# Kernel tuning notes

Measured on AMD Instinct MI355X. Metric: run time of the kernel, lower is better.

Reference implementation:

```python
import jax, jax.numpy as jnp
import numpy as np

EPS = 1e-5
B, HD, LD, OD, E = 4, 256, 512, 256, 64  # E = out_dim // reduction
H, W, H2, W2 = 64, 64, 32, 32

def conv1x1(x, Wt, b=None):
    # x: [B,C,H,W], Wt: [O,C]
    y = jnp.einsum('bchw,oc->bohw', x, Wt)
    if b is not None:
        y = y + b[None, :, None, None]
    return y

def bn(x, s, bi, m, v):
    # eval-mode BatchNorm2d with running stats
    inv = (s / jnp.sqrt(v + EPS))[None, :, None, None]
    return (x - m[None, :, None, None]) * inv + bi[None, :, None, None]

def setup_inputs() -> dict:
    key = jax.random.key(0)
    ks = jax.random.split(key, 24)
    def n(k, shape, scale=0.05):
        return jax.random.normal(k, shape, dtype=jnp.float32) * scale
    inp = {
        'high_feat': jax.random.normal(ks[0], (B, HD, H, W), dtype=jnp.float32),
        'low_feat': jax.random.normal(ks[1], (B, LD, H2, W2), dtype=jnp.float32),
        'W_high': n(ks[2], (E, HD)),
        'bn_h_scale': 1.0 + n(ks[3], (E,)), 'bn_h_bias': n(ks[4], (E,)),
        'bn_h_mean': n(ks[5], (E,)), 'bn_h_var': 0.5 + jax.random.uniform(ks[6], (E,), dtype=jnp.float32),
        'W_low': n(ks[7], (E, LD)),
        'bn_l_scale': 1.0 + n(ks[8], (E,)), 'bn_l_bias': n(ks[9], (E,)),
        'bn_l_mean': n(ks[10], (E,)), 'bn_l_var': 0.5 + jax.random.uniform(ks[11], (E,), dtype=jnp.float32),
        'W_q': n(ks[12], (E, E)), 'b_q': n(ks[13], (E,)),
        'W_k': n(ks[14], (E, E)), 'b_k': n(ks[15], (E,)),
        'W_vh': n(ks[16], (OD, HD)), 'b_vh': n(ks[17], (OD,)),
        'W_vl': n(ks[18], (OD, LD)), 'b_vl': n(ks[19], (OD,)),
        'W_out': n(ks[20], (OD, 2 * OD)),
        'bn_o_scale': 1.0 + n(ks[21], (OD,)), 'bn_o_bias': n(ks[22], (OD,)),
        'bn_o_mean': jnp.zeros((OD,), jnp.float32), 'bn_o_var': jnp.ones((OD,), jnp.float32),
        'gamma': n(ks[23], (1,), scale=0.5),
    }
    return inp

def reference(high_feat, low_feat, W_high, bn_h_scale, bn_h_bias, bn_h_mean, bn_h_var,
              W_low, bn_l_scale, bn_l_bias, bn_l_mean, bn_l_var,
              W_q, b_q, W_k, b_k, W_vh, b_vh, W_vl, b_vl,
              W_out, bn_o_scale, bn_o_bias, bn_o_mean, bn_o_var, gamma):
    N = H * W
    # bilinear upsample low_feat to high_feat spatial size (align_corners=False)
    low = jax.image.resize(low_feat, (B, LD, H, W), method='bilinear')
    he = jax.nn.relu(bn(conv1x1(high_feat, W_high), bn_h_scale, bn_h_bias, bn_h_mean, bn_h_var))
    le = jax.nn.relu(bn(conv1x1(low, W_low), bn_l_scale, bn_l_bias, bn_l_mean, bn_l_var))
    q = conv1x1(he, W_q, b_q).reshape(B, E, N)   # [B,E,N1]
    k = conv1x1(le, W_k, b_k).reshape(B, E, N)   # [B,E,N2]
    energy = jnp.einsum('bcn,bcm->bnm', q, k)    # [B,N1,N2]
    attn = jax.nn.softmax(energy, axis=-1)
    vh = conv1x1(high_feat, W_vh, b_vh).reshape(B, OD, N)
    vl = conv1x1(low, W_vl, b_vl).reshape(B, OD, N)
    out_high = jnp.einsum('bcm,bnm->bcn', vh, attn).reshape(B, OD, H, W)
    out_low = jnp.einsum('bcn,bnm->bcm', vl, attn).reshape(B, OD, H, W)
    cat = jnp.concatenate([out_high, out_low], axis=1)  # [B,2*OD,H,W]
    out = jax.nn.relu(bn(conv1x1(cat, W_out), bn_o_scale, bn_o_bias, bn_o_mean, bn_o_var))
    return high_feat + gamma[0] * out
```

## Files before the change

kernel.cpp:

```cpp
#include <hip/hip_runtime.h>
#include <hip/hip_bf16.h>

#define B_   4
#define HD_  256
#define LD_  512
#define OD_  256
#define E_   64
#define N_   4096
#define N2_  1024
#define EPS_ 1e-5f

typedef __hip_bfloat16 bf16;
typedef __attribute__((ext_vector_type(8))) short short8;
typedef __attribute__((ext_vector_type(4))) float floatx4;

#define MFMA16(a, b, c) __builtin_amdgcn_mfma_f32_16x16x32_bf16(a, b, c, 0, 0, 0)

#define GLOAD(dst, ptr) \
  asm volatile("global_load_dwordx4 %0, %1, off" : "=v"(dst) : "v"(ptr) : "memory")
#define VWAIT() do { \
  asm volatile("s_waitcnt vmcnt(0)" ::: "memory"); \
  __builtin_amdgcn_sched_barrier(0); \
} while (0)

#define WH_OFF   0
#define WL_OFF   16384
#define WQ_OFF   49152
#define WK_OFF   53248
#define WVH_OFF  57344
#define WVL_OFF  122880
#define WO_OFF   253952
#define WTOT     385024

__device__ __forceinline__ unsigned short f2b_bits(float f) {
  union { float f; unsigned int u; } cv; cv.f = f;
  unsigned int u = cv.u;
  return (unsigned short)((u + 0x7FFFu + ((u >> 16) & 1u)) >> 16);
}
__device__ __forceinline__ float bits2f(unsigned short h) {
  union { unsigned int u; float f; } cv; cv.u = ((unsigned int)h) << 16;
  return cv.f;
}
__device__ __forceinline__ float ldext(const void* p, size_t i, int fl) {
  if (fl) return __bfloat162float(((const bf16*)p)[i]);
  return ((const float*)p)[i];
}
__device__ __forceinline__ short8 ld8(const short* p) { return *(const short8*)p; }
__device__ __forceinline__ short8 i4s8(int4 v) {
  union { int4 i; short8 s; } u; u.i = v; return u.s;
}
__device__ __forceinline__ short8 ldP(const unsigned short* row, int off) {
  ushort4 a = *(const ushort4*)(row + off);
  ushort4 b = *(const ushort4*)(row + off + 4);
  short8 r;
  r[0] = (short)a.x; r[1] = (short)a.y; r[2] = (short)a.z; r[3] = (short)a.w;
  r[4] = (short)b.x; r[5] = (short)b.y; r[6] = (short)b.z; r[7] = (short)b.w;
  return r;
}

__device__ __forceinline__ size_t qk_off(int n, int e) {
  return ((size_t)(n >> 4) << 10) + ((e >> 5) << 9) + ((n & 15) << 5) + (e & 31);
}
__device__ __forceinline__ size_t v_off(int c, int m) {
  return ((size_t)(m >> 5) << 13) + ((c >> 4) << 9) + (((m >> 3) & 3) << 7)
       + ((c & 15) << 3) + (m & 7);
}
__device__ __forceinline__ size_t o_off(int n, int c) {
  return ((size_t)(n >> 4) << 12) + ((c >> 5) << 9) + ((n & 15) << 5) + (c & 31);
}

__global__ void detect_dtype_k(const void* probe, int* dflag) {
  if (threadIdx.x == 0 && blockIdx.x == 0) {
    const unsigned int* u = (const unsigned int*)probe;
    int bf = 1;
    for (int i = 0; i < 32; i++)
      if (u[i] != 0x3F803F80u) bf = 0;
    dflag[0] = bf;
  }
}

__global__ __launch_bounds__(256) void cvt_weights_k(
    const void* Wh, const void* Wl, const void* Wq, const void* Wk,
    const void* Wvh, const void* Wvl, const void* Wo,
    unsigned short* wbuf, const int* dflag)
{
  const int fl = dflag[0];
  int i = blockIdx.x * 256 + threadIdx.x;
  if (i >= WTOT) return;
  const void* src; int li;
  if      (i < WL_OFF)  { src = Wh;  li = i - WH_OFF;  }
  else if (i < WQ_OFF)  { src = Wl;  li = i - WL_OFF;  }
  else if (i < WK_OFF)  { src = Wq;  li = i - WQ_OFF;  }
  else if (i < WVH_OFF) { src = Wk;  li = i - WK_OFF;  }
  else if (i < WVL_OFF) { src = Wvh; li = i - WVH_OFF; }
  else if (i < WO_OFF)  { src = Wvl; li = i - WVL_OFF; }
  else                  { src = Wo;  li = i - WO_OFF;  }
  wbuf[i] = f2b_bits(ldext(src, li, fl));
}

__global__ __launch_bounds__(256) void transpose_cvt_k(
    const void* X, unsigned short* Xt, int C, int S, const int* dflag)
{
  __shared__ unsigned short T[64][66];
  const int fl = dflag[0];
  const int tid = threadIdx.x;
  const int s0 = blockIdx.x * 64, c0 = blockIdx.y * 64, b = blockIdx.z;
  const size_t ibase = (size_t)b * C * S;
  const size_t obase = (size_t)b * S * C;
  const int sl = tid & 63, q = tid >> 6;
  for (int i = 0; i < 16; i++) {
    int c = q + i * 4;
    T[c][sl] = f2b_bits(ldext(X, ibase + (size_t)(c0 + c) * S + s0 + sl, fl));
  }
  __syncthreads();
  for (int i = 0; i < 16; i++) {
    int s = q + i * 4;
    Xt[obase + (size_t)(s0 + s) * C + c0 + sl] = T[sl][s];
  }
}

__global__ __launch_bounds__(256) void gemm_k(
    const unsigned short* A, long sA, int lda,
    const unsigned short* Bm, long sB, int ldb,
    unsigned short* D, long sD, int ldd,
    int K, int mode, int axis, int swz,
    const void* p0, const void* p1, const void* p2, const void* p3,
    const int* dflag)
{
  const int fl = dflag[0];
  const int tid = threadIdx.x;
  const int w = tid >> 6, lane = tid & 63;
  const int g = lane >> 4, c16 = lane & 15;
  const int r0 = blockIdx.x * 64 + (w >> 1) * 32;
  const int c0 = blockIdx.y * 64 + (w & 1) * 32;
  const short* Ab = (const short*)A + (size_t)blockIdx.z * sA;
  const short* Bb = (const short*)Bm + (size_t)blockIdx.z * sB;
  unsigned short* Db = D + (size_t)blockIdx.z * sD;

  floatx4 acc[2][2];
  #pragma unroll
  for (int i = 0; i < 2; i++)
    #pragma unroll
    for (int j = 0; j < 2; j++) acc[i][j] = (floatx4){0.f, 0.f, 0.f, 0.f};

  for (int k0 = 0; k0 < K; k0 += 64) {
    short8 Af[2][2], Bf[2][2];
    #pragma unroll
    for (int t = 0; t < 2; t++)
      #pragma unroll
      for (int kc = 0; kc < 2; kc++) {
        Af[t][kc] = ld8(Ab + (size_t)(r0 + t * 16 + c16) * lda + k0 + kc * 32 + g * 8);
        Bf[t][kc] = ld8(Bb + (size_t)(c0 + t * 16 + c16) * ldb + k0 + kc * 32 + g * 8);
      }
    #pragma unroll
    for (int kc = 0; kc < 2; kc++)
      #pragma unroll
      for (int rt = 0; rt < 2; rt++)
        #pragma unroll
        for (int ct = 0; ct < 2; ct++)
          acc[rt][ct] = MFMA16(Af[rt][kc], Bf[ct][kc], acc[rt][ct]);
  }

  #pragma unroll
  for (int rt = 0; rt < 2; rt++)
    #pragma unroll
    for (int ct = 0; ct < 2; ct++)
      #pragma unroll
      for (int r = 0; r < 4; r++) {
        int rr = r0 + rt * 16 + g * 4 + r;
        int cc = c0 + ct * 16 + c16;
        int pi = axis ? rr : cc;
        float v = acc[rt][ct][r];
        if (mode == 1) v += ldext(p0, pi, fl);
        else if (mode >= 2) {
          float inv = ldext(p0, pi, fl) * rsqrtf(ldext(p3, pi, fl) + EPS_);
          v = v * inv + (ldext(p1, pi, fl) - ldext(p2, pi, fl) * inv);
          if (mode == 3) v = fmaxf(v, 0.f);
        }
        size_t idx;
        if (swz == 1)      idx = qk_off(rr, cc);
        else if (swz == 2) idx = v_off(rr, cc);
        else               idx = (size_t)rr * ldd + cc;
        Db[idx] = f2b_bits(v);
      }
}

__global__ __launch_bounds__(256) void upsample_rows_k(
    const unsigned short* src, unsigned short* dst, int relu)
{
  int idx = blockIdx.x * 256 + threadIdx.x;
  int e = idx & 63, n = (idx >> 6) & (N_ - 1), b = idx >> 18;
  int y = n >> 6, x = n & 63;
  int y0 = (y - 1) >> 1;  float wy = (y & 1) ? 0.25f : 0.75f;
  int x0 = (x - 1) >> 1;  float wx = (x & 1) ? 0.25f : 0.75f;
  int y0c = max(y0, 0), y1c = min(y0 + 1, 31);
  int x0c = max(x0, 0), x1c = min(x0 + 1, 31);
  const unsigned short* sb = src + ((size_t)b * N2_) * 64 + e;
  float v00 = bits2f(sb[(y0c * 32 + x0c) * 64]), v01 = bits2f(sb[(y0c * 32 + x1c) * 64]);
  float v10 = bits2f(sb[(y1c * 32 + x0c) * 64]), v11 = bits2f(sb[(y1c * 32 + x1c) * 64]);
  float v = (1.f - wy) * ((1.f - wx) * v00 + wx * v01)
          + wy * ((1.f - wx) * v10 + wx * v11);
  if (relu) v = fmaxf(v, 0.f);
  dst[idx] = f2b_bits(v);
}

__global__ __launch_bounds__(256) void upsample_swz_k(
    const unsigned short* src, unsigned short* dst)
{
  int idx = blockIdx.x * 256 + threadIdx.x;
  int n = idx & (N_ - 1), c = (idx >> 12) & 255, b = idx >> 20;
  int y = n >> 6, x = n & 63;
  int y0 = (y - 1) >> 1;  float wy = (y & 1) ? 0.25f : 0.75f;
  int x0 = (x - 1) >> 1;  float wx = (x & 1) ? 0.25f : 0.75f;
  int y0c = max(y0, 0), y1c = min(y0 + 1, 31);
  int x0c = max(x0, 0), x1c = min(x0 + 1, 31);
  const unsigned short* sb = src + (size_t)(b * 256 + c) * N2_;
  float v00 = bits2f(sb[y0c * 32 + x0c]), v01 = bits2f(sb[y0c * 32 + x1c]);
  float v10 = bits2f(sb[y1c * 32 + x0c]), v11 = bits2f(sb[y1c * 32 + x1c]);
  float v = (1.f - wy) * ((1.f - wx) * v00 + wx * v01)
          + wy * ((1.f - wx) * v10 + wx * v11);
  dst[(size_t)b * 256 * N_ + v_off(c, n)] = f2b_bits(v);
}


__global__ __launch_bounds__(256, 4) void attn_apply_high_mfma_k(
    const bf16* qt, const bf16* kt, const bf16* vh,
    float* lsum_p, unsigned short* ohp0, unsigned short* ohp1)
{
  __shared__ __align__(16) unsigned short Pb[2][32][132];
  __shared__ float Lw[4][32];
  const int tid = threadIdx.x;
  const int w = tid >> 6, lane = tid & 63;
  const int g = lane >> 4, c16 = lane & 15;
  const int L = blockIdx.x;
  const int b = (L & 7) >> 1;
  const int n0 = (L >> 3) * 32;
  const int half = L & 1;
  const int mbase = half * 2048, mend = mbase + 2048;
  const short* q = (const short*)qt + (size_t)b * N_ * E_;
  const short* k = (const short*)kt + (size_t)b * N_ * E_;
  const short* v = (const short*)vh + (size_t)b * OD_ * N_;

  short8 Aq[2][2];
  #pragma unroll
  for (int nt = 0; nt < 2; nt++)
    #pragma unroll
    for (int ks = 0; ks < 2; ks++)
      Aq[nt][ks] = ld8(q + qk_off(n0 + nt * 16 + c16, ks * 32 + g * 8));

  float lsum[2][4] = {};
  floatx4 oacc[2][4];
  #pragma unroll
  for (int nt = 0; nt < 2; nt++)
    #pragma unroll
    for (int ct = 0; ct < 4; ct++)
      oacc[nt][ct] = (floatx4){0.f, 0.f, 0.f, 0.f};

  short8 BkC[2][2];
  #pragma unroll
  for (int mt = 0; mt < 2; mt++)
    #pragma unroll
    for (int ks = 0; ks < 2; ks++)
      BkC[mt][ks] = ld8(k + qk_off(mbase + w * 32 + mt * 16 + c16, ks * 32 + g * 8));

  int buf = 0;
  for (int m0 = mbase; m0 < mend; m0 += 128, buf ^= 1) {
    int4 bv[8];
    #pragma unroll
    for (int ks = 0; ks < 2; ks++)
      #pragma unroll
      for (int ct = 0; ct < 4; ct++)
        GLOAD(bv[ks * 4 + ct],
              (v + v_off(w * 64 + ct * 16 + c16, m0 + ks * 32 + g * 8)));
    floatx4 s[2][2];
    #pragma unroll
    for (int nt = 0; nt < 2; nt++)
      #pragma unroll
      for (int mt = 0; mt < 2; mt++) {
        floatx4 z = (floatx4){0.f, 0.f, 0.f, 0.f};
        z = MFMA16(Aq[nt][0], BkC[mt][0], z);
        z = MFMA16(Aq[nt][1], BkC[mt][1], z);
        s[nt][mt] = z;
      }
    int mn_ = m0 + 128;
    if (mn_ < mend) {
      #pragma unroll
      for (int mt = 0; mt < 2; mt++)
        #pragma unroll
        for (int ks = 0; ks < 2; ks++)
          BkC[mt][ks] = ld8(k + qk_off(mn_ + w * 32 + mt * 16 + c16, ks * 32 + g * 8));
    }
    #pragma unroll
    for (int nt = 0; nt < 2; nt++)
      #pragma unroll
      for (int mt = 0; mt < 2; mt++)
        #pragma unroll
        for (int r = 0; r < 4; r++) {
          float p = __expf(fminf(s[nt][mt][r], 60.f));
          lsum[nt][r] += p;
          Pb[buf][nt * 16 + g * 4 + r][w * 32 + mt * 16 + c16] = f2b_bits(p);
        }
    __syncthreads();
    VWAIT();
    #pragma unroll
    for (int ks = 0; ks < 2; ks++) {
      short8 Ap0 = ldP(&Pb[buf][c16][0],      ks * 32 + g * 8);
      short8 Ap1 = ldP(&Pb[buf][16 + c16][0], ks * 32 + g * 8);
      #pragma unroll
      for (int ct = 0; ct < 4; ct++) {
        short8 Bv = i4s8(bv[ks * 4 + ct]);
        oacc[0][ct] = MFMA16(Ap0, Bv, oacc[0][ct]);
        oacc[1][ct] = MFMA16(Ap1, Bv, oacc[1][ct]);
      }
    }
    #pragma unroll
    for (int ks = 0; ks < 2; ks++)
      #pragma unroll
      for (int ct = 0; ct < 4; ct++)
        GLOAD(bv[ks * 4 + ct],
              (v + v_off(w * 64 + ct * 16 + c16, m0 + (ks + 2) * 32 + g * 8)));
    VWAIT();
    #pragma unroll
    for (int ks = 0; ks < 2; ks++) {
      short8 Ap0 = ldP(&Pb[buf][c16][0],      (ks + 2) * 32 + g * 8);
      short8 Ap1 = ldP(&Pb[buf][16 + c16][0], (ks + 2) * 32 + g * 8);
      #pragma unroll
      for (int ct = 0; ct < 4; ct++) {
        short8 Bv = i4s8(bv[ks * 4 + ct]);
        oacc[0][ct] = MFMA16(Ap0, Bv, oacc[0][ct]);
        oacc[1][ct] = MFMA16(Ap1, Bv, oacc[1][ct]);
      }
    }
  }
  #pragma unroll
  for (int d = 1; d < 16; d <<= 1)
    #pragma unroll
    for (int nt = 0; nt < 2; nt++)
      #pragma unroll
      for (int r = 0; r < 4; r++)
        lsum[nt][r] += __shfl_xor(lsum[nt][r], d);
  if (c16 == 0)
    #pragma unroll
    for (int nt = 0; nt < 2; nt++)
      #pragma unroll
      for (int r = 0; r < 4; r++)
        Lw[w][nt * 16 + g * 4 + r] = lsum[nt][r];
  __syncthreads();
  if (tid < 32)
    lsum_p[(size_t)half * 16384 + (size_t)b * N_ + n0 + tid] =
        Lw[0][tid] + Lw[1][tid] + Lw[2][tid] + Lw[3][tid];
  unsigned short* op = (half ? ohp1 : ohp0) + (size_t)b * N_ * OD_;
  #pragma unroll
  for (int nt = 0; nt < 2; nt++)
    #pragma unroll
    for (int ct = 0; ct < 4; ct++)
      #pragma unroll
      for (int r = 0; r < 4; r++) {
        int n = n0 + nt * 16 + g * 4 + r;
        int c = w * 64 + ct * 16 + c16;
        op[o_off(n, c)] = f2b_bits(oacc[nt][ct][r]);
      }
}

__global__ __launch_bounds__(256) void reduce_high_k(
    const unsigned short* p0, const unsigned short* p1, const float* lsum_p,
    unsigned short* oh, float* rsumG)
{
  size_t i8 = ((size_t)blockIdx.x * 256 + threadIdx.x) * 8;
  int slab = (int)(i8 >> 20);
  int loc  = (int)(i8 & 0xFFFFF);
  int n = (loc >> 12) * 16 + ((loc >> 5) & 15);
  int row = slab * N_ + n;
  float l = lsum_p[row] + lsum_p[16384 + row];
  float ri = 1.0f / l;
  const unsigned short* a = p0 + i8;
  const unsigned short* b = p1 + i8;
  short8 o;
  #pragma unroll
  for (int i = 0; i < 8; i++)
    o[i] = (short)f2b_bits((bits2f(a[i]) + bits2f(b[i])) * ri);
  *(short8*)(oh + i8) = o;
  if ((loc & 31) == 0) rsumG[row] = l;
}

__global__ __launch_bounds__(256, 4) void attn_apply_low_mfma_k(
    const bf16* qt, const bf16* kt, const bf16* vl,
    const float* rsumG, unsigned short* olp0, unsigned short* olp1)
{
  __shared__ __align__(16) unsigned short Pb[2][32][132];
  const int tid = threadIdx.x;
  const int w = tid >> 6, lane = tid & 63;
  const int g = lane >> 4, c16 = lane & 15;
  const int L = blockIdx.x;
  const int b = (L & 7) >> 1;
  const int m0 = (L >> 3) * 32;
  const int half = L & 1;
  const int nbase = half * 2048, nend = nbase + 2048;
  const short* q = (const short*)qt + (size_t)b * N_ * E_;
  const short* k = (const short*)kt + (size_t)b * N_ * E_;
  const short* v = (const short*)vl + (size_t)b * OD_ * N_;

  short8 Ak[2][2];
  #pragma unroll
  for (int mt = 0; mt < 2; mt++)
    #pragma unroll
    for (int ks = 0; ks < 2; ks++)
      Ak[mt][ks] = ld8(k + qk_off(m0 + mt * 16 + c16, ks * 32 + g * 8));

  floatx4 oacc[2][4];
  #pragma unroll
  for (int mt = 0; mt < 2; mt++)
    #pragma unroll
    for (int ct = 0; ct < 4; ct++)
      oacc[mt][ct] = (floatx4){0.f, 0.f, 0.f, 0.f};

  short8 BqC[2][2];
  float riC[2];
  #pragma unroll
  for (int nt = 0; nt < 2; nt++) {
    #pragma unroll
    for (int ks = 0; ks < 2; ks++)
      BqC[nt][ks] = ld8(q + qk_off(nbase + w * 32 + nt * 16 + c16, ks * 32 + g * 8));
    riC[nt] = 1.0f / rsumG[(size_t)b * N_ + nbase + w * 32 + nt * 16 + c16];
  }

  int buf = 0;
  for (int nL = nbase; nL < nend; nL += 128, buf ^= 1) {
    int4 bv[8];
    #pragma unroll
    for (int ks = 0; ks < 2; ks++)
      #pragma unroll
      for (int ct = 0; ct < 4; ct++)
        GLOAD(bv[ks * 4 + ct],
              (v + v_off(w * 64 + ct * 16 + c16, nL + ks * 32 + g * 8)));
    floatx4 s[2][2];
    #pragma unroll
    for (int mt = 0; mt < 2; mt++)
      #pragma unroll
      for (int nt = 0; nt < 2; nt++) {
        floatx4 z = (floatx4){0.f, 0.f, 0.f, 0.f};
        z = MFMA16(Ak[mt][0], BqC[nt][0], z);
        z = MFMA16(Ak[mt][1], BqC[nt][1], z);
        s[mt][nt] = z;
      }
    float riU[2]; riU[0] = riC[0]; riU[1] = riC[1];
    int nn_ = nL + 128;
    if (nn_ < nend) {
      #pragma unroll
      for (int nt = 0; nt < 2; nt++) {
        #pragma unroll
        for (int ks = 0; ks < 2; ks++)
          BqC[nt][ks] = ld8(q + qk_off(nn_ + w * 32 + nt * 16 + c16, ks * 32 + g * 8));
        riC[nt] = 1.0f / rsumG[(size_t)b * N_ + nn_ + w * 32 + nt * 16 + c16];
      }
    }
    #pragma unroll
    for (int mt = 0; mt < 2; mt++)
      #pragma unroll
      for (int nt = 0; nt < 2; nt++)
        #pragma unroll
        for (int r = 0; r < 4; r++)
          Pb[buf][mt * 16 + g * 4 + r][w * 32 + nt * 16 + c16] =
              f2b_bits(__expf(fminf(s[mt][nt][r], 60.f)) * riU[nt]);
    __syncthreads();
    VWAIT();
    #pragma unroll
    for (int ks = 0; ks < 2; ks++) {
      short8 Ap0 = ldP(&Pb[buf][c16][0],      ks * 32 + g * 8);
      short8 Ap1 = ldP(&Pb[buf][16 + c16][0], ks * 32 + g * 8);
      #pragma unroll
      for (int ct = 0; ct < 4; ct++) {
        short8 Bv = i4s8(bv[ks * 4 + ct]);
        oacc[0][ct] = MFMA16(Ap0, Bv, oacc[0][ct]);
        oacc[1][ct] = MFMA16(Ap1, Bv, oacc[1][ct]);
      }
    }
    #pragma unroll
    for (int ks = 0; ks < 2; ks++)
      #pragma unroll
      for (int ct = 0; ct < 4; ct++)
        GLOAD(bv[ks * 4 + ct],
              (v + v_off(w * 64 + ct * 16 + c16, nL + (ks + 2) * 32 + g * 8)));
    VWAIT();
    #pragma unroll
    for (int ks = 0; ks < 2; ks++) {
      short8 Ap0 = ldP(&Pb[buf][c16][0],      (ks + 2) * 32 + g * 8);
      short8 Ap1 = ldP(&Pb[buf][16 + c16][0], (ks + 2) * 32 + g * 8);
      #pragma unroll
      for (int ct = 0; ct < 4; ct++) {
        short8 Bv = i4s8(bv[ks * 4 + ct]);
        oacc[0][ct] = MFMA16(Ap0, Bv, oacc[0][ct]);
        oacc[1][ct] = MFMA16(Ap1, Bv, oacc[1][ct]);
      }
    }
  }
  unsigned short* op = (half ? olp1 : olp0) + (size_t)b * N_ * OD_;
  #pragma unroll
  for (int mt = 0; mt < 2; mt++)
    #pragma unroll
    for (int ct = 0; ct < 4; ct++)
      #pragma unroll
      for (int r = 0; r < 4; r++) {
        int m = m0 + mt * 16 + g * 4 + r;
        int c = w * 64 + ct * 16 + c16;
        op[o_off(m, c)] = f2b_bits(oacc[mt][ct][r]);
      }
}

__global__ __launch_bounds__(256) void reduce_low_k(
    const unsigned short* p0, const unsigned short* p1, unsigned short* ol)
{
  size_t i8 = ((size_t)blockIdx.x * 256 + threadIdx.x) * 8;
  const unsigned short* a = p0 + i8;
  const unsigned short* b = p1 + i8;
  short8 o;
  #pragma unroll
  for (int i = 0; i < 8; i++)
    o[i] = (short)f2b_bits(bits2f(a[i]) + bits2f(b[i]));
  *(short8*)(ol + i8) = o;
}

__global__ __launch_bounds__(256) void final_mfma_k(
    const unsigned short* Wo, const unsigned short* oh, const unsigned short* ol,
    const void* sc, const void* bi, const void* mn, const void* vr,
    const void* hf, const void* gamma, void* out, const int* dflag)
{
  const int fl = dflag[0];
  const int tid = threadIdx.x;
  const int w = tid >> 6, lane = tid & 63;
  const int g = lane >> 4, c16 = lane & 15;
  const int r0 = blockIdx.x * 64 + (w >> 1) * 32;
  const int c0 = blockIdx.y * 64 + (w & 1) * 32;
  const int b = blockIdx.z;

  floatx4 acc[2][2];
  #pragma unroll
  for (int i = 0; i < 2; i++)
    #pragma unroll
    for (int j = 0; j < 2; j++) acc[i][j] = (floatx4){0.f, 0.f, 0.f, 0.f};

  #pragma unroll
  for (int half = 0; half < 2; half++) {
    const short* Bb = (const short*)(half ? ol : oh) + (size_t)b * N_ * 256;
    for (int k0 = 0; k0 < 256; k0 += 64) {
      short8 Af[2][2], Bf[2][2];
      #pragma unroll
      for (int t = 0; t < 2; t++)
        #pragma unroll
        for (int kc = 0; kc < 2; kc++) {
          Af[t][kc] = ld8((const short*)Wo + (size_t)(r0 + t * 16 + c16) * 512 +
                          half * 256 + k0 + kc * 32 + g * 8);
          Bf[t][kc] = ld8(Bb + o_off(c0 + t * 16 + c16, k0 + kc * 32 + g * 8));
        }
      #pragma unroll
      for (int kc = 0; kc < 2; kc++)
        #pragma unroll
        for (int rt = 0; rt < 2; rt++)
          #pragma unroll
          for (int ct = 0; ct < 2; ct++)
            acc[rt][ct] = MFMA16(Af[rt][kc], Bf[ct][kc], acc[rt][ct]);
    }
  }

  float gm = ldext(gamma, 0, fl);
  #pragma unroll
  for (int rt = 0; rt < 2; rt++)
    #pragma unroll
    for (int r = 0; r < 4; r++) {
      int o = r0 + rt * 16 + g * 4 + r;
      float inv = ldext(sc, o, fl) * rsqrtf(ldext(vr, o, fl) + EPS_);
      float bb = ldext(bi, o, fl) - ldext(mn, o, fl) * inv;
      #pragma unroll
      for (int ct = 0; ct < 2; ct++) {
        int n = c0 + ct * 16 + c16;
        float v = acc[rt][ct][r] * inv + bb;
        v = fmaxf(v, 0.f);
        size_t idx = ((size_t)b * OD_ + o) * N_ + n;
        float res = ldext(hf, idx, fl) + gm * v;
        if (fl) ((bf16*)out)[idx] = __float2bfloat16(res);
        else    ((float*)out)[idx] = res;
      }
    }
}

extern "C" void kernel_launch(void* const* d_in, const int* in_sizes, int n_in,
                              void* d_out, int out_size, void* d_ws, size_t ws_size,
                              hipStream_t stream)
{
  const void* hf     = d_in[0];
  const void* lf     = d_in[1];
  const void* W_high = d_in[2];
  const void* bhs = d_in[3],  *bhb = d_in[4],  *bhm = d_in[5],  *bhv = d_in[6];
  const void* W_low  = d_in[7];
  const void* bls = d_in[8],  *blb = d_in[9],  *blm = d_in[10], *blv = d_in[11];
  const void* W_q    = d_in[12], *b_q = d_in[13];
  const void* W_k    = d_in[14], *b_k = d_in[15];
  const void* W_vh   = d_in[16], *b_vh = d_in[17];
  const void* W_vl   = d_in[18], *b_vl = d_in[19];
  const void* W_out  = d_in[20];
  const void* bos = d_in[21], *bob = d_in[22], *bom = d_in[23], *bov = d_in[24];
  const void* gamma  = d_in[25];

  char* wp = (char*)d_ws;
  int*   dflag  = (int*)wp;                                 wp += 64;
  float* rsum   = (float*)wp;                               wp += 16384 * 4;
  float* lsum_p = (float*)wp;                               wp += 2 * 16384 * 4;
  unsigned short* wbuf  = (unsigned short*)wp;              wp += WTOT * 2;
  unsigned short* hf_t  = (unsigned short*)wp;              wp += (size_t)B_ * N_ * 256 * 2;
  unsigned short* lf_t  = (unsigned short*)wp;              wp += (size_t)B_ * N2_ * 512 * 2;
  unsigned short* he_t  = (unsigned short*)wp;              wp += (size_t)B_ * N_ * 64 * 2;
  unsigned short* le_sm = (unsigned short*)wp;              wp += (size_t)B_ * N2_ * 64 * 2;
  unsigned short* le_t  = (unsigned short*)wp;              wp += (size_t)B_ * N_ * 64 * 2;
  unsigned short* vl_sm = (unsigned short*)wp;              wp += (size_t)B_ * 256 * N2_ * 2;
  unsigned short* vh    = (unsigned short*)wp;              wp += (size_t)B_ * 256 * N_ * 2;
  unsigned short* vl    = (unsigned short*)wp;              wp += (size_t)B_ * 256 * N_ * 2;
  unsigned short* ol    = (unsigned short*)wp;              wp += (size_t)B_ * N_ * 256 * 2;
  unsigned short* pext  = (unsigned short*)wp;              wp += (size_t)B_ * N_ * 256 * 2;
  unsigned short* oh = hf_t;
  unsigned short* qv = lf_t;
  unsigned short* kv = lf_t + (size_t)B_ * N_ * 64;
  unsigned short* ohp0 = ol;
  unsigned short* ohp1 = pext;
  unsigned short* olp0 = vh;
  unsigned short* olp1 = pext;

  dim3 blk(256);
  detect_dtype_k<<<1, 64, 0, stream>>>(bov, dflag);
  cvt_weights_k<<<WTOT / 256, blk, 0, stream>>>(W_high, W_low, W_q, W_k, W_vh, W_vl, W_out,
                                                wbuf, dflag);
  transpose_cvt_k<<<dim3(64, 4, B_), blk, 0, stream>>>(hf, hf_t, 256, N_, dflag);
  transpose_cvt_k<<<dim3(16, 8, B_), blk, 0, stream>>>(lf, lf_t, 512, N2_, dflag);

  gemm_k<<<dim3(256, 1, 1), blk, 0, stream>>>(hf_t, 0, 256, wbuf + WH_OFF, 0, 256,
      he_t, 0, 64, 256, 3, 0, 0, bhs, bhb, bhm, bhv, dflag);
  gemm_k<<<dim3(4, 64, B_), blk, 0, stream>>>(wbuf + WVH_OFF, 0, 256,
      hf_t, (long)N_ * 256, 256, vh, (long)256 * N_, N_, 256, 1, 1, 2,
      b_vh, b_vh, b_vh, b_vh, dflag);
  gemm_k<<<dim3(64, 1, 1), blk, 0, stream>>>(lf_t, 0, 512, wbuf + WL_OFF, 0, 512,
      le_sm, 0, 64, 512, 2, 0, 0, bls, blb, blm, blv, dflag);
  gemm_k<<<dim3(4, 16, B_), blk, 0, stream>>>(wbuf + WVL_OFF, 0, 512,
      lf_t, (long)N2_ * 512, 512, vl_sm, (long)256 * N2_, N2_, 512, 1, 1, 0,
      b_vl, b_vl, b_vl, b_vl, dflag);
  upsample_rows_k<<<(B_ * N_ * 64) / 256, blk, 0, stream>>>(le_sm, le_t, 1);
  upsample_swz_k <<<(B_ * 256 * N_) / 256, blk, 0, stream>>>(vl_sm, vl);
  gemm_k<<<dim3(256, 1, 1), blk, 0, stream>>>(he_t, 0, 64, wbuf + WQ_OFF, 0, 64,
      qv, 0, 64, 64, 1, 0, 1, b_q, b_q, b_q, b_q, dflag);
  gemm_k<<<dim3(256, 1, 1), blk, 0, stream>>>(le_t, 0, 64, wbuf + WK_OFF, 0, 64,
      kv, 0, 64, 64, 1, 0, 1, b_k, b_k, b_k, b_k, dflag);

  attn_apply_high_mfma_k<<<dim3(1024), blk, 0, stream>>>((const bf16*)qv, (const bf16*)kv,
      (const bf16*)vh, lsum_p, ohp0, ohp1);
  reduce_high_k<<<dim3(2048), blk, 0, stream>>>(ohp0, ohp1, lsum_p, oh, rsum);
  attn_apply_low_mfma_k <<<dim3(1024), blk, 0, stream>>>((const bf16*)qv, (const bf16*)kv,
      (const bf16*)vl, rsum, olp0, olp1);
  reduce_low_k<<<dim3(2048), blk, 0, stream>>>(olp0, olp1, ol);

  final_mfma_k<<<dim3(4, 64, B_), blk, 0, stream>>>(wbuf + WO_OFF, oh, ol,
      bos, bob, bom, bov, hf, gamma, d_out, dflag);
}
```

Baseline: 399.1 us.

## Store all GEMM operands in MFMA fragment-tiled layout

Introduces a generic fragment-tiled layout (16-row by 32-k tiles stored contiguously) and uses it for the converted weights, the transposed inputs, the upsampled key features, the intermediate he tensor and the final-stage operands. Every gemm and MFMA kernel now loads operands through this layout, so each wave's 16-byte fragment loads hit contiguous memory rather than strided rows. The cost is scattered stores in the producer kernels (weight conversion, transpose, upsample) and more index arithmetic. It also risks layout mismatches between producers and consumers, such as le_sm, which is still written row-major and read by the upsample kernel.

```diff
diff --git a/kernel.cpp b/kernel.cpp
--- a/kernel.cpp
+++ b/kernel.cpp
@@ -58,15 +58,13 @@
   return r;
 }
 
-__device__ __forceinline__ size_t qk_off(int n, int e) {
-  return ((size_t)(n >> 4) << 10) + ((e >> 5) << 9) + ((n & 15) << 5) + (e & 31);
+__device__ __forceinline__ size_t frag_off(int r, int k, int K) {
+  return ((size_t)(r >> 4) * ((size_t)K << 4)) + ((size_t)(k >> 5) << 9)
+       + ((r & 15) << 5) + (k & 31);
 }
 __device__ __forceinline__ size_t v_off(int c, int m) {
   return ((size_t)(m >> 5) << 13) + ((c >> 4) << 9) + (((m >> 3) & 3) << 7)
        + ((c & 15) << 3) + (m & 7);
-}
-__device__ __forceinline__ size_t o_off(int n, int c) {
-  return ((size_t)(n >> 4) << 12) + ((c >> 5) << 9) + ((n & 15) << 5) + (c & 31);
 }
 
 __global__ void detect_dtype_k(const void* probe, int* dflag) {
@@ -87,15 +85,17 @@
   const int fl = dflag[0];
   int i = blockIdx.x * 256 + threadIdx.x;
   if (i >= WTOT) return;
-  const void* src; int li;
-  if      (i < WL_OFF)  { src = Wh;  li = i - WH_OFF;  }
-  else if (i < WQ_OFF)  { src = Wl;  li = i - WL_OFF;  }
-  else if (i < WK_OFF)  { src = Wq;  li = i - WQ_OFF;  }
-  else if (i < WVH_OFF) { src = Wk;  li = i - WK_OFF;  }
-  else if (i < WVL_OFF) { src = Wvh; li = i - WVH_OFF; }
-  else if (i < WO_OFF)  { src = Wvl; li = i - WVL_OFF; }
-  else                  { src = Wo;  li = i - WO_OFF;  }
-  wbuf[i] = f2b_bits(ldext(src, li, fl));
+  const void* src; int li, off, ksh;
+  if      (i < WL_OFF)  { src = Wh;  li = i - WH_OFF;  off = WH_OFF;  ksh = 8; }
+  else if (i < WQ_OFF)  { src = Wl;  li = i - WL_OFF;  off = WL_OFF;  ksh = 9; }
+  else if (i < WK_OFF)  { src = Wq;  li = i - WQ_OFF;  off = WQ_OFF;  ksh = 6; }
+  else if (i < WVH_OFF) { src = Wk;  li = i - WK_OFF;  off = WK_OFF;  ksh = 6; }
+  else if (i < WVL_OFF) { src = Wvh; li = i - WVH_OFF; off = WVH_OFF; ksh = 8; }
+  else if (i < WO_OFF)  { src = Wvl; li = i - WVL_OFF; off = WVL_OFF; ksh = 9; }
+  else                  { src = Wo;  li = i - WO_OFF;  off = WO_OFF;  ksh = 9; }
+  int K = 1 << ksh;
+  int r = li >> ksh, k = li & (K - 1);
+  wbuf[off + frag_off(r, k, K)] = f2b_bits(ldext(src, li, fl));
 }
 
 __global__ __launch_bounds__(256) void transpose_cvt_k(
@@ -115,13 +115,13 @@
   __syncthreads();
   for (int i = 0; i < 16; i++) {
     int s = q + i * 4;
-    Xt[obase + (size_t)(s0 + s) * C + c0 + sl] = T[sl][s];
+    Xt[obase + frag_off(s0 + s, c0 + sl, C)] = T[sl][s];
   }
 }
 
 __global__ __launch_bounds__(256) void gemm_k(
-    const unsigned short* A, long sA, int lda,
-    const unsigned short* Bm, long sB, int ldb,
+    const unsigned short* A, long sA,
+    const unsigned short* Bm, long sB,
     unsigned short* D, long sD, int ldd,
     int K, int mode, int axis, int swz,
     const void* p0, const void* p1, const void* p2, const void* p3,
@@ -149,8 +149,8 @@
     for (int t = 0; t < 2; t++)
       #pragma unroll
       for (int kc = 0; kc < 2; kc++) {
-        Af[t][kc] = ld8(Ab + (size_t)(r0 + t * 16 + c16) * lda + k0 + kc * 32 + g * 8);
-        Bf[t][kc] = ld8(Bb + (size_t)(c0 + t * 16 + c16) * ldb + k0 + kc * 32 + g * 8);
+        Af[t][kc] = ld8(Ab + frag_off(r0 + t * 16 + c16, k0 + kc * 32 + g * 8, K));
+        Bf[t][kc] = ld8(Bb + frag_off(c0 + t * 16 + c16, k0 + kc * 32 + g * 8, K));
       }
     #pragma unroll
     for (int kc = 0; kc < 2; kc++)
@@ -178,7 +178,7 @@
           if (mode == 3) v = fmaxf(v, 0.f);
         }
         size_t idx;
-        if (swz == 1)      idx = qk_off(rr, cc);
+        if (swz == 1)      idx = frag_off(rr, cc, ldd);
         else if (swz == 2) idx = v_off(rr, cc);
         else               idx = (size_t)rr * ldd + cc;
         Db[idx] = f2b_bits(v);
@@ -201,7 +201,7 @@
   float v = (1.f - wy) * ((1.f - wx) * v00 + wx * v01)
           + wy * ((1.f - wx) * v10 + wx * v11);
   if (relu) v = fmaxf(v, 0.f);
-  dst[idx] = f2b_bits(v);
+  dst[(size_t)b * N_ * 64 + frag_off(n, e, 64)] = f2b_bits(v);
 }
 
 __global__ __launch_bounds__(256) void upsample_swz_k(
@@ -246,7 +246,7 @@
   for (int nt = 0; nt < 2; nt++)
     #pragma unroll
     for (int ks = 0; ks < 2; ks++)
-      Aq[nt][ks] = ld8(q + qk_off(n0 + nt * 16 + c16, ks * 32 + g * 8));
+      Aq[nt][ks] = ld8(q + frag_off(n0 + nt * 16 + c16, ks * 32 + g * 8, 64));
 
   float lsum[2][4] = {};
   floatx4 oacc[2][4];
@@ -261,7 +261,7 @@
   for (int mt = 0; mt < 2; mt++)
     #pragma unroll
     for (int ks = 0; ks < 2; ks++)
-      BkC[mt][ks] = ld8(k + qk_off(mbase + w * 32 + mt * 16 + c16, ks * 32 + g * 8));
+      BkC[mt][ks] = ld8(k + frag_off(mbase + w * 32 + mt * 16 + c16, ks * 32 + g * 8, 64));
 
   int buf = 0;
   for (int m0 = mbase; m0 < mend; m0 += 128, buf ^= 1) {
@@ -288,7 +288,7 @@
       for (int mt = 0; mt < 2; mt++)
         #pragma unroll
         for (int ks = 0; ks < 2; ks++)
-          BkC[mt][ks] = ld8(k + qk_off(mn_ + w * 32 + mt * 16 + c16, ks * 32 + g * 8));
+          BkC[mt][ks] = ld8(k + frag_off(mn_ + w * 32 + mt * 16 + c16, ks * 32 + g * 8, 64));
     }
     #pragma unroll
     for (int nt = 0; nt < 2; nt++)
@@ -358,7 +358,7 @@
       for (int r = 0; r < 4; r++) {
         int n = n0 + nt * 16 + g * 4 + r;
         int c = w * 64 + ct * 16 + c16;
-        op[o_off(n, c)] = f2b_bits(oacc[nt][ct][r]);
+        op[frag_off(n, c, 256)] = f2b_bits(oacc[nt][ct][r]);
       }
 }
 
@@ -405,7 +405,7 @@
   for (int mt = 0; mt < 2; mt++)
     #pragma unroll
     for (int ks = 0; ks < 2; ks++)
-      Ak[mt][ks] = ld8(k + qk_off(m0 + mt * 16 + c16, ks * 32 + g * 8));
+      Ak[mt][ks] = ld8(k + frag_off(m0 + mt * 16 + c16, ks * 32 + g * 8, 64));
 
   floatx4 oacc[2][4];
   #pragma unroll
@@ -420,7 +420,7 @@
   for (int nt = 0; nt < 2; nt++) {
     #pragma unroll
     for (int ks = 0; ks < 2; ks++)
-      BqC[nt][ks] = ld8(q + qk_off(nbase + w * 32 + nt * 16 + c16, ks * 32 + g * 8));
+      BqC[nt][ks] = ld8(q + frag_off(nbase + w * 32 + nt * 16 + c16, ks * 32 + g * 8, 64));
     riC[nt] = 1.0f / rsumG[(size_t)b * N_ + nbase + w * 32 + nt * 16 + c16];
   }
 
@@ -450,7 +450,7 @@
       for (int nt = 0; nt < 2; nt++) {
         #pragma unroll
         for (int ks = 0; ks < 2; ks++)
-          BqC[nt][ks] = ld8(q + qk_off(nn_ + w * 32 + nt * 16 + c16, ks * 32 + g * 8));
+          BqC[nt][ks] = ld8(q + frag_off(nn_ + w * 32 + nt * 16 + c16, ks * 32 + g * 8, 64));
         riC[nt] = 1.0f / rsumG[(size_t)b * N_ + nn_ + w * 32 + nt * 16 + c16];
       }
     }
@@ -503,7 +503,7 @@
       for (int r = 0; r < 4; r++) {
         int m = m0 + mt * 16 + g * 4 + r;
         int c = w * 64 + ct * 16 + c16;
-        op[o_off(m, c)] = f2b_bits(oacc[mt][ct][r]);
+        op[frag_off(m, c, 256)] = f2b_bits(oacc[mt][ct][r]);
       }
 }
 
@@ -548,9 +548,9 @@
       for (int t = 0; t < 2; t++)
         #pragma unroll
         for (int kc = 0; kc < 2; kc++) {
-          Af[t][kc] = ld8((const short*)Wo + (size_t)(r0 + t * 16 + c16) * 512 +
-                          half * 256 + k0 + kc * 32 + g * 8);
-          Bf[t][kc] = ld8(Bb + o_off(c0 + t * 16 + c16, k0 + kc * 32 + g * 8));
+          Af[t][kc] = ld8((const short*)Wo + frag_off(r0 + t * 16 + c16,
+                          half * 256 + k0 + kc * 32 + g * 8, 512));
+          Bf[t][kc] = ld8(Bb + frag_off(c0 + t * 16 + c16, k0 + kc * 32 + g * 8, 256));
         }
       #pragma unroll
       for (int kc = 0; kc < 2; kc++)
@@ -631,21 +631,21 @@
   transpose_cvt_k<<<dim3(64, 4, B_), blk, 0, stream>>>(hf, hf_t, 256, N_, dflag);
   transpose_cvt_k<<<dim3(16, 8, B_), blk, 0, stream>>>(lf, lf_t, 512, N2_, dflag);
 
-  gemm_k<<<dim3(256, 1, 1), blk, 0, stream>>>(hf_t, 0, 256, wbuf + WH_OFF, 0, 256,
-      he_t, 0, 64, 256, 3, 0, 0, bhs, bhb, bhm, bhv, dflag);
-  gemm_k<<<dim3(4, 64, B_), blk, 0, stream>>>(wbuf + WVH_OFF, 0, 256,
-      hf_t, (long)N_ * 256, 256, vh, (long)256 * N_, N_, 256, 1, 1, 2,
+  gemm_k<<<dim3(256, 1, 1), blk, 0, stream>>>(hf_t, 0, wbuf + WH_OFF, 0,
+      he_t, 0, 64, 256, 3, 0, 1, bhs, bhb, bhm, bhv, dflag);
+  gemm_k<<<dim3(4, 64, B_), blk, 0, stream>>>(wbuf + WVH_OFF, 0,
+      hf_t, (long)N_ * 256, vh, (long)256 * N_, N_, 256, 1, 1, 2,
       b_vh, b_vh, b_vh, b_vh, dflag);
-  gemm_k<<<dim3(64, 1, 1), blk, 0, stream>>>(lf_t, 0, 512, wbuf + WL_OFF, 0, 512,
+  gemm_k<<<dim3(64, 1, 1), blk, 0, stream>>>(lf_t, 0, wbuf + WL_OFF, 0,
       le_sm, 0, 64, 512, 2, 0, 0, bls, blb, blm, blv, dflag);
-  gemm_k<<<dim3(4, 16, B_), blk, 0, stream>>>(wbuf + WVL_OFF, 0, 512,
-      lf_t, (long)N2_ * 512, 512, vl_sm, (long)256 * N2_, N2_, 512, 1, 1, 0,
+  gemm_k<<<dim3(4, 16, B_), blk, 0, stream>>>(wbuf + WVL_OFF, 0,
+      lf_t, (long)N2_ * 512, vl_sm, (long)256 * N2_, N2_, 512, 1, 1, 0,
       b_vl, b_vl, b_vl, b_vl, dflag);
   upsample_rows_k<<<(B_ * N_ * 64) / 256, blk, 0, stream>>>(le_sm, le_t, 1);
   upsample_swz_k <<<(B_ * 256 * N_) / 256, blk, 0, stream>>>(vl_sm, vl);
-  gemm_k<<<dim3(256, 1, 1), blk, 0, stream>>>(he_t, 0, 64, wbuf + WQ_OFF, 0, 64,
+  gemm_k<<<dim3(256, 1, 1), blk, 0, stream>>>(he_t, 0, wbuf + WQ_OFF, 0,
       qv, 0, 64, 64, 1, 0, 1, b_q, b_q, b_q, b_q, dflag);
-  gemm_k<<<dim3(256, 1, 1), blk, 0, stream>>>(le_t, 0, 64, wbuf + WK_OFF, 0, 64,
+  gemm_k<<<dim3(256, 1, 1), blk, 0, stream>>>(le_t, 0, wbuf + WK_OFF, 0,
       kv, 0, 64, 64, 1, 0, 1, b_k, b_k, b_k, b_k, dflag);
 
   attn_apply_high_mfma_k<<<dim3(1024), blk, 0, stream>>>((const bf16*)qv, (const bf16*)kv,
```

Result: faster. 381.1 us (-4.5%).
